# Performance work log

Measured on AMD Instinct MI355X. Metric: run time of the kernel, lower is better.

The kernel has to match this reference:

```python
import jax, jax.numpy as jnp
import numpy as np

H, TH, NH, NL, NB = 512, 768, 8, 12, 2
NE, NU, NI, NNZ, K, B = 16000, 2000, 4000, 40000, 10, 64
MD = H // 2
GAMA = 0.1


def _prelu(x, a):
    return jnp.where(x >= 0, x, a * x)


def _spmm(r, c, v, X, n):
    # sparse [n, m] @ X: gather X rows by col index, scale, segment-sum by row.
    return jax.ops.segment_sum(v[:, None] * X[c], r, num_segments=n)


def _forward(systemid, adj_row, adj_col, itemid_set,
             token_embeds, adj_val, node_embeds, user_embedding,
             token_proj_w, token_proj_b, trans_w, trans_b, trans_t_w, trans_t_b,
             meta_w1, meta_b1, meta_w2, meta_b2, sim_w1, sim_w2,
             p1_w1, p1_b1, p1_w2, p1_b2, p2_w, p2_b, prelu_a):
    tok = token_embeds @ token_proj_w + token_proj_b               # [B, H]
    # grouped mean over rows sharing the same system id (vectorized segment-mean)
    same = (systemid[:, None] == systemid[None, :]).astype(tok.dtype)
    group_mean = (same @ tok) / same.sum(1, keepdims=True)         # [B, H]
    filt = _prelu(group_mean @ trans_w + trans_b, prelu_a) * group_mean
    h = jax.nn.relu(filt @ meta_w1 + meta_b1)
    mapping = (h @ meta_w2 + meta_b2).reshape(B, H, H)             # per-sample hypernet weights
    enhanced = jnp.einsum('bh,bhk->bk', user_embedding[systemid], mapping)
    all_tok = user_embedding.at[systemid].set(enhanced)            # [NU, H]
    tok_edge = jnp.zeros_like(user_embedding).at[systemid].set(group_mean)
    # similarity between (enhanced) user/token reps and item reps
    u_rep = all_tok @ sim_w1
    i_rep = node_embeds[itemid_set] @ sim_w2
    u_n = u_rep / jnp.maximum(jnp.linalg.norm(u_rep, axis=1, keepdims=True), 1e-12)
    i_n = i_rep / jnp.maximum(jnp.linalg.norm(i_rep, axis=1, keepdims=True), 1e-12)
    sim = jax.nn.sigmoid(u_n @ i_n.T)                              # [NU, NI]
    tv, ti = jax.lax.top_k(sim, K)
    # combined sparse adjacency = original COO + per-user top-k added edges
    rows = jnp.concatenate([adj_row, jnp.repeat(jnp.arange(NU), K)])
    cols = jnp.concatenate([adj_col, itemid_set[ti].reshape(-1)])
    vals = jnp.concatenate([adj_val, tv.reshape(-1)])
    v_u = vals / jax.ops.segment_sum(vals, rows, num_segments=NU)[rows]   # row-normalized user->item
    v_i = vals / jax.ops.segment_sum(vals, cols, num_segments=NE)[cols]   # row-normalized item->user
    # LightGCN-style 2-layer propagation with multiplicative token gating
    user_tok = _prelu(tok_edge @ trans_t_w + trans_t_b, prelu_a) * tok_edge
    u0, i0 = all_tok, node_embeds
    Ai0 = _spmm(rows, cols, v_u, i0, NU)
    u1 = Ai0 + Ai0 * user_tok
    Att = _spmm(cols, rows, v_i, user_tok, NE)
    i1 = _spmm(cols, rows, v_i, u0, NE) + Att * i0
    Ai1 = _spmm(rows, cols, v_u, i1, NU)
    u2 = Ai1 + Ai1 * user_tok
    i2 = _spmm(cols, rows, v_i, u1, NE) + Att * i1
    user_final = (u0 + u1 + u2) / 3.0
    item_final = (i0 + i1 + i2) / 3.0
    # reconstruction loss vs dense adjacency restricted to item columns
    inv = jnp.full((NE,), -1, jnp.int32).at[itemid_set].set(jnp.arange(NI, dtype=jnp.int32))
    icol = inv[adj_col]
    valid = (icol >= 0).astype(sim.dtype)
    dense = jnp.zeros((NU, NI), sim.dtype).at[adj_row, jnp.maximum(icol, 0)].add(adj_val * valid)
    loss = GAMA * jnp.mean((sim - dense) ** 2)
    # prefix-prompt projection from per-batch system embeddings
    sys_final = user_final[systemid][:, None, :]                   # [B, 1, H]
    p1 = jax.nn.relu(sys_final @ p1_w1 + p1_b1) @ p1_w2 + p1_b2 + sys_final
    p2 = p1 @ p2_w + p2_b
    prompt = p2.reshape(B, 1, NL, NB, NH, H // NH).transpose(2, 3, 0, 4, 1, 5)
    return prompt, item_final, loss


def setup_inputs():
    ks = jax.random.split(jax.random.key(0), 20)
    rng = np.random.default_rng(0)
    s = 0.02
    itemid_set = jnp.asarray(np.sort(rng.choice(NE, NI, replace=False)).astype(np.int32))
    user_embedding = (s * jax.random.normal(ks[4], (NU, H), jnp.float32)).at[0].set(0.0)
    return {
        'systemid': jax.random.randint(ks[0], (B,), 0, NU),
        'adj_row': jax.random.randint(ks[1], (NNZ,), 0, NU),
        'adj_col': jax.random.randint(ks[2], (NNZ,), 0, NE),
        'itemid_set': itemid_set,
        'token_embeds': jax.random.normal(ks[3], (B, TH), jnp.float32),
        'adj_val': jnp.ones((NNZ,), jnp.float32),
        'node_embeds': s * jax.random.normal(ks[5], (NE, H), jnp.float32),
        'user_embedding': user_embedding,
        'token_proj_w': s * jax.random.normal(ks[6], (TH, H), jnp.float32),
        'token_proj_b': jnp.zeros((H,), jnp.float32),
        'trans_w': s * jax.random.normal(ks[7], (H, H), jnp.float32),
        'trans_b': jnp.zeros((H,), jnp.float32),
        'trans_t_w': s * jax.random.normal(ks[8], (H, H), jnp.float32),
        'trans_t_b': jnp.zeros((H,), jnp.float32),
        'meta_w1': s * jax.random.normal(ks[9], (H, MD), jnp.float32),
        'meta_b1': jnp.zeros((MD,), jnp.float32),
        'meta_w2': s * jax.random.normal(ks[10], (MD, H * H), jnp.float32),
        'meta_b2': jnp.zeros((H * H,), jnp.float32),
        'sim_w1': jax.random.normal(ks[11], (H, H), jnp.float32),
        'sim_w2': jax.random.normal(ks[12], (H, H), jnp.float32),
        'p1_w1': s * jax.random.normal(ks[13], (H, MD), jnp.float32),
        'p1_b1': jnp.zeros((MD,), jnp.float32),
        'p1_w2': s * jax.random.normal(ks[14], (MD, H), jnp.float32),
        'p1_b2': jnp.zeros((H,), jnp.float32),
        'p2_w': s * jax.random.normal(ks[15], (H, NL * NB * H), jnp.float32),
        'p2_b': jnp.zeros((NL * NB * H,), jnp.float32),
        'prelu_a': jnp.array(0.25, jnp.float32),
    }


def reference(systemid, adj_row, adj_col, itemid_set, token_embeds, adj_val,
              node_embeds, user_embedding, token_proj_w, token_proj_b,
              trans_w, trans_b, trans_t_w, trans_t_b,
              meta_w1, meta_b1, meta_w2, meta_b2, sim_w1, sim_w2,
              p1_w1, p1_b1, p1_w2, p1_b2, p2_w, p2_b, prelu_a):
    return _forward(systemid, adj_row, adj_col, itemid_set, token_embeds, adj_val,
                    node_embeds, user_embedding, token_proj_w, token_proj_b,
                    trans_w, trans_b, trans_t_w, trans_t_b,
                    meta_w1, meta_b1, meta_w2, meta_b2, sim_w1, sim_w2,
                    p1_w1, p1_b1, p1_w2, p1_b2, p2_w, p2_b, prelu_a)
```

## Files before the change

### kernel.cpp

```cpp
#include <hip/hip_runtime.h>

#define H     512
#define THD   768
#define MDIM  256
#define NE    16000
#define NU    2000
#define NI    4000
#define NNZ   40000
#define KTOP  10
#define NBATCH 64
#define NEDGE 60000
#define GAMA  0.1f
#define P2N   12288
#define PROMPT_N 786432
#define NLOSSB 2048

__device__ __forceinline__ float sigmoidf(float x){ return 1.0f/(1.0f+expf(-x)); }
__device__ __forceinline__ float4 f4z(){ return make_float4(0.f,0.f,0.f,0.f); }

__device__ __forceinline__ void gll16(const float* g, float* l){
  __builtin_amdgcn_global_load_lds(
      (const __attribute__((address_space(1))) void*)g,
      (__attribute__((address_space(3))) void*)l, 16, 0, 0);
}

__global__ void k_tok(const float* __restrict__ A, const float* __restrict__ W,
                      const float* __restrict__ bias, float* __restrict__ C){
  int b=blockIdx.x, c=blockIdx.y*256+threadIdx.x;
  const float* a=A+b*THD; float s=bias[c];
  for(int k=0;k<THD;k++) s+=a[k]*W[k*H+c];
  C[b*H+c]=s;
}

__global__ void k_gm(const int* __restrict__ sysid, const float* __restrict__ tok,
                     float* __restrict__ gm){
  int b=blockIdx.x, c=blockIdx.y*256+threadIdx.x;
  int sid=sysid[b]; float s=0.f, cnt=0.f;
  for(int j=0;j<NBATCH;j++){ if(sysid[j]==sid){ s+=tok[j*H+c]; cnt+=1.f; } }
  gm[b*H+c]=s/cnt;
}

__global__ __launch_bounds__(512) void k_front(const int* __restrict__ sysid,
        const float* __restrict__ gm,
        const float* __restrict__ trans_w, const float* __restrict__ trans_b,
        const float* __restrict__ mw1, const float* __restrict__ mb1,
        const float* __restrict__ ue, const float* __restrict__ mb2,
        const float* __restrict__ trt_w, const float* __restrict__ trt_b,
        const float* __restrict__ pa,
        float* __restrict__ hh, float* __restrict__ ueT, float* __restrict__ enh,
        float* __restrict__ usertok){
  __shared__ float fl[512];
  __shared__ float hp[512];
  int b=blockIdx.x, t=threadIdx.x, which=blockIdx.y;
  if(which==0){
    const float* g=gm+b*H;
    float s=trans_b[t];
    for(int k=0;k<H;k++) s+=g[k]*trans_w[k*H+t];
    float al=pa[0]; float pr=(s>=0.f)? s : al*s;
    fl[t]=pr*g[t];
    __syncthreads();
    int m=t&255, half=t>>8;
    float s2=0.f; int k0=half*256;
    for(int k=0;k<256;k++) s2+=fl[k0+k]*mw1[(k0+k)*MDIM+m];
    hp[t]=s2;
    __syncthreads();
    if(t<256) hh[b*MDIM+t]=fmaxf(hp[t]+hp[t+256]+mb1[t],0.f);
  } else if(which==1){
    const float* u=ue+(size_t)sysid[b]*H;
    float v=u[t];
    ueT[t*64+b]=v;
    float s=0.f;
    for(int h=0;h<H;h++) s+=u[h]*mb2[(size_t)h*H+t];
    enh[b*H+t]=s;
  } else {
    const float* a=gm+b*H; float s=trt_b[t];
    for(int k=0;k<H;k++) s+=a[k]*trt_w[k*H+t];
    float al=pa[0]; float pr=(s>=0.f)? s : al*s;
    usertok[(size_t)sysid[b]*H+t]=pr*gm[b*H+t];
  }
}

#define HCH 8
__global__ __launch_bounds__(128) void k_big(const float* __restrict__ hh,
        const float* __restrict__ ueT, const float* __restrict__ w2,
        float* __restrict__ partials){
  __shared__ float a_lds[2][HCH][64];
  __shared__ float w_lds[2][HCH][256];
  int m=blockIdx.x;
  int kt=blockIdx.y&1, hs=blockIdx.y>>1;
  int k0=kt*256;
  int hbase=hs*256;
  int t=threadIdx.x;
  int kg=t&15, bg=t>>4;
  const float* w2m = w2 + (size_t)m*(size_t)(H*H);

  float4 acc[8][4];
  #pragma unroll
  for(int r=0;r<8;r++){
    #pragma unroll
    for(int c=0;c<4;c++) acc[r][c]=f4z();
  }

  #define STAGE(buf,hc) do{                                             \
    int h0=hbase+(hc)*HCH;                                              \
    gll16(ueT + (size_t)(h0+(t>>4))*64 + (t&15)*4,                      \
          &a_lds[buf][t>>4][(t&15)*4]);                                 \
    _Pragma("unroll")                                                   \
    for(int j=0;j<4;j++){                                               \
      int i=t+j*128;                                                    \
      gll16(w2m + (size_t)(h0+(i>>6))*H + k0 + (i&63)*4,                \
            &w_lds[buf][i>>6][(i&63)*4]);                               \
    }                                                                   \
  }while(0)

  STAGE(0,0);
  int cur=0;
  for(int hc=0;hc<32;hc++){
    __syncthreads();
    if(hc<31) STAGE(cur^1,hc+1);
    #pragma unroll
    for(int hl=0;hl<HCH;hl++){
      float4 aL=*(const float4*)&a_lds[cur][hl][bg*4];
      float4 aH=*(const float4*)&a_lds[cur][hl][32+bg*4];
      float4 w0=*(const float4*)&w_lds[cur][hl][kg*4];
      float4 w1=*(const float4*)&w_lds[cur][hl][64+kg*4];
      float4 w2v=*(const float4*)&w_lds[cur][hl][128+kg*4];
      float4 w3=*(const float4*)&w_lds[cur][hl][192+kg*4];
      #define FMA4(ac,av,wv) ac.x+=(av)*wv.x; ac.y+=(av)*wv.y; ac.z+=(av)*wv.z; ac.w+=(av)*wv.w;
      #define ROWC(r,av) FMA4(acc[r][0],av,w0) FMA4(acc[r][1],av,w1) FMA4(acc[r][2],av,w2v) FMA4(acc[r][3],av,w3)
      ROWC(0,aL.x) ROWC(1,aL.y) ROWC(2,aL.z) ROWC(3,aL.w)
      ROWC(4,aH.x) ROWC(5,aH.y) ROWC(6,aH.z) ROWC(7,aH.w)
      #undef ROWC
      #undef FMA4
    }
    cur^=1;
  }
  int slice=hs*256+m;
  #pragma unroll
  for(int r=0;r<8;r++){
    int br=(r<4)? (bg*4+r) : (32+bg*4+(r-4));
    float hv=hh[br*MDIM+m];
    float* p=partials+((size_t)slice*NBATCH+br)*H+k0+kg*4;
    *(float4*)(p)    =make_float4(acc[r][0].x*hv,acc[r][0].y*hv,acc[r][0].z*hv,acc[r][0].w*hv);
    *(float4*)(p+64) =make_float4(acc[r][1].x*hv,acc[r][1].y*hv,acc[r][1].z*hv,acc[r][1].w*hv);
    *(float4*)(p+128)=make_float4(acc[r][2].x*hv,acc[r][2].y*hv,acc[r][2].z*hv,acc[r][2].w*hv);
    *(float4*)(p+192)=make_float4(acc[r][3].x*hv,acc[r][3].y*hv,acc[r][3].z*hv,acc[r][3].w*hv);
  }
  #undef STAGE
}

__global__ void k_red1(const float* __restrict__ partials, float* __restrict__ partial2){
  int idx=blockIdx.x*256+threadIdx.x;
  int g=idx>>15, col=idx&32767;
  const float* p=partials+(size_t)g*16*32768+col;
  float s=0.f;
  #pragma unroll
  for(int m=0;m<16;m++) s+=p[(size_t)m*32768];
  partial2[idx]=s;
}
__global__ void k_red2s(const int* __restrict__ sysid, const float* __restrict__ partial2,
                        const float* __restrict__ enh, float* __restrict__ alltok){
  int idx=blockIdx.x*256+threadIdx.x;
  int b=idx>>9, k=idx&511;
  float s=enh[idx];
  #pragma unroll
  for(int g=0;g<32;g++) s+=partial2[(size_t)g*32768+idx];
  alltok[(size_t)sysid[b]*H+k]=s;
}

template<int EPI, bool NT, bool AIDX>
__device__ __forceinline__ void gemm_body(float (*As)[68], float (*Bs)[68],
        const float* __restrict__ A, const float* __restrict__ Bm,
        const float* __restrict__ bias, const int* __restrict__ aidx,
        float* __restrict__ C, int M, int N, int K, int bx, int by){
  int n0=bx*64, m0=by*64;
  int t=threadIdx.x;
  int tn=t&15, tm=t>>4;
  float4 pa[2], pb[2];
  #pragma unroll
  for(int i=0;i<2;i++){
    int idx=t+i*256; int r=idx>>3, q=idx&7;
    int grow=m0+r;
    pa[i]=f4z();
    if(grow<M){
      const float* arow=A+(size_t)(AIDX? aidx[grow]:grow)*K;
      pa[i]=*(const float4*)(arow+q*4);
    }
  }
  #pragma unroll
  for(int i=0;i<2;i++){
    if(!NT){
      int idx=t+i*256; int r=idx>>4, q=idx&15;
      pb[i]=*(const float4*)(Bm+(size_t)r*N+n0+q*4);
    } else {
      int idx=t+i*256; int r=idx>>3, q=idx&7;
      int gn=n0+r;
      pb[i]=f4z();
      if(gn<N) pb[i]=*(const float4*)(Bm+(size_t)gn*K+q*4);
    }
  }
  float acc[4][4]={};
  for(int kt=0;kt<K;kt+=32){
    __syncthreads();
    #pragma unroll
    for(int i=0;i<2;i++){
      int idx=t+i*256; int r=idx>>3, q=idx&7;
      As[q*4+0][r]=pa[i].x; As[q*4+1][r]=pa[i].y; As[q*4+2][r]=pa[i].z; As[q*4+3][r]=pa[i].w;
    }
    #pragma unroll
    for(int i=0;i<2;i++){
      if(!NT){
        int idx=t+i*256; int r=idx>>4, q=idx&15;
        *(float4*)&Bs[r][q*4]=pb[i];
      } else {
        int idx=t+i*256; int r=idx>>3, q=idx&7;
        Bs[q*4+0][r]=pb[i].x; Bs[q*4+1][r]=pb[i].y; Bs[q*4+2][r]=pb[i].z; Bs[q*4+3][r]=pb[i].w;
      }
    }
    __syncthreads();
    if(kt+32<K){
      #pragma unroll
      for(int i=0;i<2;i++){
        int idx=t+i*256; int r=idx>>3, q=idx&7;
        int grow=m0+r;
        pa[i]=f4z();
        if(grow<M){
          const float* arow=A+(size_t)(AIDX? aidx[grow]:grow)*K;
          pa[i]=*(const float4*)(arow+kt+32+q*4);
        }
      }
      #pragma unroll
      for(int i=0;i<2;i++){
        if(!NT){
          int idx=t+i*256; int r=idx>>4, q=idx&15;
          pb[i]=*(const float4*)(Bm+(size_t)(kt+32+r)*N+n0+q*4);
        } else {
          int idx=t+i*256; int r=idx>>3, q=idx&7;
          int gn=n0+r;
          pb[i]=f4z();
          if(gn<N) pb[i]=*(const float4*)(Bm+(size_t)gn*K+kt+32+q*4);
        }
      }
    }
    #pragma unroll 8
    for(int k=0;k<32;k++){
      float4 a4=*(const float4*)&As[k][tm*4];
      float4 b4=*(const float4*)&Bs[k][tn*4];
      acc[0][0]+=a4.x*b4.x; acc[0][1]+=a4.x*b4.y; acc[0][2]+=a4.x*b4.z; acc[0][3]+=a4.x*b4.w;
      acc[1][0]+=a4.y*b4.x; acc[1][1]+=a4.y*b4.y; acc[1][2]+=a4.y*b4.z; acc[1][3]+=a4.y*b4.w;
      acc[2][0]+=a4.z*b4.x; acc[2][1]+=a4.z*b4.y; acc[2][2]+=a4.z*b4.z; acc[2][3]+=a4.z*b4.w;
      acc[3][0]+=a4.w*b4.x; acc[3][1]+=a4.w*b4.y; acc[3][2]+=a4.w*b4.z; acc[3][3]+=a4.w*b4.w;
    }
  }
  #pragma unroll
  for(int bi=0;bi<4;bi++){
    int row=m0+tm*4+bi; if(row>=M) continue;
    #pragma unroll
    for(int ki=0;ki<4;ki++){
      int col=n0+tn*4+ki; if(col>=N) continue;
      float v=acc[bi][ki];
      if(EPI==0){ if(bias) v+=bias[col]; }
      else { v=sigmoidf(v); }
      C[(size_t)row*N+col]=v;
    }
  }
}

template<int EPI, bool NT, bool AIDX>
__global__ __launch_bounds__(256) void k_gemm(const float* __restrict__ A,
        const float* __restrict__ Bm, const float* __restrict__ bias,
        const int* __restrict__ aidx, float* __restrict__ C, int M, int N, int K){
  __shared__ float As[32][68];
  __shared__ float Bs[32][68];
  gemm_body<EPI,NT,AIDX>(As,Bs,A,Bm,bias,aidx,C,M,N,K,blockIdx.x,blockIdx.y);
}

__global__ __launch_bounds__(256) void k_gemm_ui(const float* __restrict__ alltok,
        const float* __restrict__ node_emb, const float* __restrict__ sw1,
        const float* __restrict__ sw2, const int* __restrict__ itemid,
        float* __restrict__ urep, float* __restrict__ irep){
  __shared__ float As[32][68];
  __shared__ float Bs[32][68];
  if(blockIdx.y<32)
    gemm_body<0,false,false>(As,Bs,alltok,sw1,nullptr,nullptr,urep,NU,H,H,blockIdx.x,blockIdx.y);
  else
    gemm_body<0,false,true >(As,Bs,node_emb,sw2,nullptr,itemid,irep,NI,H,H,blockIdx.x,blockIdx.y-32);
}

__global__ __launch_bounds__(512) void k_gemm_sim(const float* __restrict__ A,
        const float* __restrict__ Bm, float* __restrict__ C, int M, int N){
  __shared__ float As[32][132];
  __shared__ float Bs[32][260];
  int n0=blockIdx.x*256, m0=blockIdx.y*128;
  int t=threadIdx.x;
  int tn=t&31, tm=t>>5;
  float4 pa[2], pb[4];
  #pragma unroll
  for(int i=0;i<2;i++){
    int idx=t+i*512; int r=idx>>3, q=idx&7;
    pa[i]=f4z();
    if(m0+r<M) pa[i]=*(const float4*)(A+(size_t)(m0+r)*H+q*4);
  }
  #pragma unroll
  for(int i=0;i<4;i++){
    int idx=t+i*512; int r=idx>>3, q=idx&7;
    pb[i]=f4z();
    if(n0+r<N) pb[i]=*(const float4*)(Bm+(size_t)(n0+r)*H+q*4);
  }
  float4 acc[8][2];
  #pragma unroll
  for(int r=0;r<8;r++){ acc[r][0]=f4z(); acc[r][1]=f4z(); }
  for(int kt=0;kt<H;kt+=32){
    __syncthreads();
    #pragma unroll
    for(int i=0;i<2;i++){
      int idx=t+i*512; int r=idx>>3, q=idx&7;
      As[q*4+0][r]=pa[i].x; As[q*4+1][r]=pa[i].y; As[q*4+2][r]=pa[i].z; As[q*4+3][r]=pa[i].w;
    }
    #pragma unroll
    for(int i=0;i<4;i++){
      int idx=t+i*512; int r=idx>>3, q=idx&7;
      Bs[q*4+0][r]=pb[i].x; Bs[q*4+1][r]=pb[i].y; Bs[q*4+2][r]=pb[i].z; Bs[q*4+3][r]=pb[i].w;
    }
    __syncthreads();
    if(kt+32<H){
      #pragma unroll
      for(int i=0;i<2;i++){
        int idx=t+i*512; int r=idx>>3, q=idx&7;
        pa[i]=f4z();
        if(m0+r<M) pa[i]=*(const float4*)(A+(size_t)(m0+r)*H+kt+32+q*4);
      }
      #pragma unroll
      for(int i=0;i<4;i++){
        int idx=t+i*512; int r=idx>>3, q=idx&7;
        pb[i]=f4z();
        if(n0+r<N) pb[i]=*(const float4*)(Bm+(size_t)(n0+r)*H+kt+32+q*4);
      }
    }
    #pragma unroll 8
    for(int k=0;k<32;k++){
      float4 a0=*(const float4*)&As[k][tm*4];
      float4 a1=*(const float4*)&As[k][64+tm*4];
      float4 b0=*(const float4*)&Bs[k][tn*4];
      float4 b1=*(const float4*)&Bs[k][128+tn*4];
      #define FMA4(ac,av,bv) ac.x+=(av)*bv.x; ac.y+=(av)*bv.y; ac.z+=(av)*bv.z; ac.w+=(av)*bv.w;
      #define ROW(r,av) FMA4(acc[r][0],av,b0) FMA4(acc[r][1],av,b1)
      ROW(0,a0.x) ROW(1,a0.y) ROW(2,a0.z) ROW(3,a0.w)
      ROW(4,a1.x) ROW(5,a1.y) ROW(6,a1.z) ROW(7,a1.w)
      #undef ROW
      #undef FMA4
    }
  }
  #pragma unroll
  for(int r=0;r<8;r++){
    int row=m0+((r<4)? (tm*4+r) : (64+tm*4+(r-4)));
    if(row>=M) continue;
    #pragma unroll
    for(int c=0;c<2;c++){
      int col0=n0+c*128+tn*4;
      float vv[4]={acc[r][c].x,acc[r][c].y,acc[r][c].z,acc[r][c].w};
      #pragma unroll
      for(int j=0;j<4;j++){
        int col=col0+j;
        if(col<N) C[(size_t)row*N+col]=sigmoidf(vv[j]);
      }
    }
  }
}

__global__ __launch_bounds__(256) void k_rownorm2(float* __restrict__ U, float* __restrict__ I){
  int r=blockIdx.x, t=threadIdx.x;
  float* X=(r<NU)? U+(size_t)r*H : I+(size_t)(r-NU)*H;
  float v1=X[t], v2=X[t+256];
  float ss=v1*v1+v2*v2;
  for(int o=32;o;o>>=1) ss+=__shfl_xor(ss,o);
  __shared__ float red[4];
  if((t&63)==0) red[t>>6]=ss;
  __syncthreads();
  float tot=red[0]+red[1]+red[2]+red[3];
  float nrm=fmaxf(sqrtf(tot),1e-12f);
  X[t]=v1/nrm; X[t+256]=v2/nrm;
}

__global__ __launch_bounds__(256) void k_topk(const float* __restrict__ sim,
        float* __restrict__ tv, int* __restrict__ ti){
  __shared__ float rv[4];
  __shared__ int   ri[4];
  int u=blockIdx.x, t=threadIdx.x;
  float v[16];
  #pragma unroll
  for(int j=0;j<16;j++){
    int gi=t+j*256;
    v[j]=(gi<NI)? sim[(size_t)u*NI+gi] : -1e30f;
  }
  for(int k=0;k<KTOP;k++){
    float bv=-1e30f; int bi=1<<30;
    #pragma unroll
    for(int j=0;j<16;j++){
      int gi=t+j*256;
      if(v[j]>bv){ bv=v[j]; bi=gi; }
    }
    #pragma unroll
    for(int o=32;o;o>>=1){
      float ov=__shfl_xor(bv,o); int oi=__shfl_xor(bi,o);
      if(ov>bv || (ov==bv && oi<bi)){ bv=ov; bi=oi; }
    }
    if((t&63)==0){ rv[t>>6]=bv; ri[t>>6]=bi; }
    __syncthreads();
    float fv=rv[0]; int fi=ri[0];
    #pragma unroll
    for(int w=1;w<4;w++){
      float ov=rv[w]; int oi=ri[w];
      if(ov>fv || (ov==fv && oi<fi)){ fv=ov; fi=oi; }
    }
    if(t==0){ tv[u*KTOP+k]=fv; ti[u*KTOP+k]=fi; }
    int jj=fi>>8, tt=fi&255;
    #pragma unroll
    for(int j=0;j<16;j++) if(tt==t && j==jj) v[j]=-1e30f;
    __syncthreads();
  }
}

__global__ void k_edges(const int* __restrict__ adj_row, const int* __restrict__ adj_col,
        const float* __restrict__ adj_val, const int* __restrict__ itemid,
        const float* __restrict__ tv, const int* __restrict__ ti,
        int* __restrict__ rows, int* __restrict__ cols, float* __restrict__ vals,
        float* __restrict__ seg_r, float* __restrict__ seg_c,
        int* __restrict__ row_cnt, int* __restrict__ col_cnt, int* __restrict__ inv){
  int e=blockIdx.x*256+threadIdx.x; if(e>=NEDGE) return;
  if(e<NI) inv[itemid[e]]=e;
  int r,c; float v;
  if(e<NNZ){ r=adj_row[e]; c=adj_col[e]; v=adj_val[e]; }
  else { int x=e-NNZ; int u=x/KTOP; r=u; c=itemid[ti[x]]; v=tv[x]; }
  rows[e]=r; cols[e]=c; vals[e]=v;
  atomicAdd(&seg_r[r],v); atomicAdd(&seg_c[c],v);
  atomicAdd(&row_cnt[r],1); atomicAdd(&col_cnt[c],1);
}

__global__ __launch_bounds__(1024) void k_scan(const int* __restrict__ rc, int* __restrict__ rp,
        const int* __restrict__ cc, int* __restrict__ cp){
  const int* cnt; int* ptr; int n;
  if(blockIdx.x==0){ cnt=rc; ptr=rp; n=NU; } else { cnt=cc; ptr=cp; n=NE; }
  int t=threadIdx.x;
  int chunk=(n+1023)>>10;
  int base=t*chunk;
  int s=0;
  for(int i=0;i<chunk;i++){ int j=base+i; if(j<n) s+=cnt[j]; }
  __shared__ int buf[1024];
  buf[t]=s; __syncthreads();
  for(int off=1;off<1024;off<<=1){
    int y=(t>=off)? buf[t-off]:0;
    __syncthreads();
    buf[t]+=y;
    __syncthreads();
  }
  int run=buf[t]-s;
  for(int i=0;i<chunk;i++){ int j=base+i; if(j<n){ ptr[j]=run; run+=cnt[j]; } }
  if(t==1023) ptr[n]=buf[1023];
}

__global__ void k_fill(const int* __restrict__ rows, const int* __restrict__ cols,
        const float* __restrict__ vals,
        const int* __restrict__ row_ptr, const int* __restrict__ col_ptr,
        const float* __restrict__ seg_r, const float* __restrict__ seg_c,
        int* __restrict__ fr, int* __restrict__ fc,
        int* __restrict__ ebr, int* __restrict__ ebc,
        float* __restrict__ v_u, float* __restrict__ v_i,
        const int* __restrict__ inv, float* __restrict__ dense){
  int e=blockIdx.x*256+threadIdx.x; if(e>=NEDGE) return;
  int r=rows[e], c=cols[e];
  ebr[row_ptr[r]+atomicAdd(&fr[r],1)]=e;
  ebc[col_ptr[c]+atomicAdd(&fc[c],1)]=e;
  v_u[e]=vals[e]/seg_r[r];
  v_i[e]=vals[e]/seg_c[c];
  if(e<NNZ){
    int ic=inv[c];
    if(ic>=0) atomicAdd(&dense[(size_t)r*NI+ic],vals[e]);
  }
}

__device__ __forceinline__ void spmm_u_body(int u, const int* __restrict__ row_ptr,
        const int* __restrict__ ebr, const int* __restrict__ cols,
        const float* __restrict__ v_u, const float* __restrict__ X,
        const float* __restrict__ usertok, float* __restrict__ out,
        int* sc, float* sv, float (*red)[512]){
  int t=threadIdx.x, w=t>>6, l=t&63;
  int s=row_ptr[u], n=row_ptr[u+1]-s;
  float4 a0=f4z(), a1=f4z();
  for(int base=0;base<n;base+=128){
    int cnt=min(n-base,128);
    if(t<cnt){ int e=ebr[s+base+t]; sc[t]=cols[e]; sv[t]=v_u[e]; }
    __syncthreads();
    for(int j=w;j<cnt;j+=4){
      float v=sv[j];
      const float4* xr=(const float4*)(X+(size_t)sc[j]*H);
      float4 x0=xr[l], x1=xr[l+64];
      a0.x+=v*x0.x; a0.y+=v*x0.y; a0.z+=v*x0.z; a0.w+=v*x0.w;
      a1.x+=v*x1.x; a1.y+=v*x1.y; a1.z+=v*x1.z; a1.w+=v*x1.w;
    }
    __syncthreads();
  }
  if(w>0){ *(float4*)&red[w-1][l*4]=a0; *(float4*)&red[w-1][l*4+256]=a1; }
  __syncthreads();
  if(w==0){
    #pragma unroll
    for(int ww=0;ww<3;ww++){
      float4 r0=*(const float4*)&red[ww][l*4], r1=*(const float4*)&red[ww][l*4+256];
      a0.x+=r0.x; a0.y+=r0.y; a0.z+=r0.z; a0.w+=r0.w;
      a1.x+=r1.x; a1.y+=r1.y; a1.z+=r1.z; a1.w+=r1.w;
    }
    const float4* ut=(const float4*)(usertok+(size_t)u*H);
    float4 u0=ut[l], u1=ut[l+64];
    float4* o=(float4*)(out+(size_t)u*H);
    o[l]   =make_float4(a0.x+a0.x*u0.x, a0.y+a0.y*u0.y, a0.z+a0.z*u0.z, a0.w+a0.w*u0.w);
    o[l+64]=make_float4(a1.x+a1.x*u1.x, a1.y+a1.y*u1.y, a1.z+a1.z*u1.z, a1.w+a1.w*u1.w);
  }
}

__device__ __forceinline__ void spmm_i1_body(int ib, const int* __restrict__ col_ptr,
        const int* __restrict__ ebc, const int* __restrict__ rows,
        const float* __restrict__ v_i, const float* __restrict__ alltok,
        const float* __restrict__ usertok, const float* __restrict__ i0,
        float* __restrict__ Att, float* __restrict__ i1){
  int i=ib*4+(threadIdx.x>>6);
  int l=threadIdx.x&63;
  int s=col_ptr[i], e1=col_ptr[i+1];
  float4 aA0=f4z(),aA1=f4z(),aU0=f4z(),aU1=f4z();
  for(int j=s;j<e1;j++){
    int e=ebc[j]; float v=v_i[e]; int r=rows[e];
    const float4* ur=(const float4*)(usertok+(size_t)r*H);
    const float4* ar=(const float4*)(alltok+(size_t)r*H);
    float4 u0=ur[l],u1v=ur[l+64],A0=ar[l],A1=ar[l+64];
    aA0.x+=v*u0.x; aA0.y+=v*u0.y; aA0.z+=v*u0.z; aA0.w+=v*u0.w;
    aA1.x+=v*u1v.x; aA1.y+=v*u1v.y; aA1.z+=v*u1v.z; aA1.w+=v*u1v.w;
    aU0.x+=v*A0.x; aU0.y+=v*A0.y; aU0.z+=v*A0.z; aU0.w+=v*A0.w;
    aU1.x+=v*A1.x; aU1.y+=v*A1.y; aU1.z+=v*A1.z; aU1.w+=v*A1.w;
  }
  size_t o=(size_t)i*128;
  const float4* z=(const float4*)i0;
  float4 z0=z[o+l], z1=z[o+l+64];
  ((float4*)Att)[o+l]   =aA0;
  ((float4*)Att)[o+l+64]=aA1;
  ((float4*)i1)[o+l]   =make_float4(aU0.x+aA0.x*z0.x, aU0.y+aA0.y*z0.y, aU0.z+aA0.z*z0.z, aU0.w+aA0.w*z0.w);
  ((float4*)i1)[o+l+64]=make_float4(aU1.x+aA1.x*z1.x, aU1.y+aA1.y*z1.y, aU1.z+aA1.z*z1.z, aU1.w+aA1.w*z1.w);
}

__device__ __forceinline__ void spmm_i2_body(int ib, const int* __restrict__ col_ptr,
        const int* __restrict__ ebc, const int* __restrict__ rows,
        const float* __restrict__ v_i, const float* __restrict__ u1,
        const float* __restrict__ Att, const float* __restrict__ i1,
        const float* __restrict__ i0, float* __restrict__ item_out){
  int i=ib*4+(threadIdx.x>>6);
  int l=threadIdx.x&63;
  int s=col_ptr[i], e1=col_ptr[i+1];
  float4 a0=f4z(), a1=f4z();
  for(int j=s;j<e1;j++){
    int e=ebc[j]; float v=v_i[e];
    const float4* ur=(const float4*)(u1+(size_t)rows[e]*H);
    float4 x0=ur[l], x1=ur[l+64];
    a0.x+=v*x0.x; a0.y+=v*x0.y; a0.z+=v*x0.z; a0.w+=v*x0.w;
    a1.x+=v*x1.x; a1.y+=v*x1.y; a1.z+=v*x1.z; a1.w+=v*x1.w;
  }
  size_t o=(size_t)i*128;
  float4 A0=((const float4*)Att)[o+l], A1=((const float4*)Att)[o+l+64];
  float4 I0=((const float4*)i1)[o+l],  I1=((const float4*)i1)[o+l+64];
  float4 Z0=((const float4*)i0)[o+l],  Z1=((const float4*)i0)[o+l+64];
  float4 r0=make_float4((Z0.x+I0.x+a0.x+A0.x*I0.x)/3.f,(Z0.y+I0.y+a0.y+A0.y*I0.y)/3.f,
                        (Z0.z+I0.z+a0.z+A0.z*I0.z)/3.f,(Z0.w+I0.w+a0.w+A0.w*I0.w)/3.f);
  float4 r1=make_float4((Z1.x+I1.x+a1.x+A1.x*I1.x)/3.f,(Z1.y+I1.y+a1.y+A1.y*I1.y)/3.f,
                        (Z1.z+I1.z+a1.z+A1.z*I1.z)/3.f,(Z1.w+I1.w+a1.w+A1.w*I1.w)/3.f);
  ((float4*)item_out)[o+l]=r0;
  ((float4*)item_out)[o+l+64]=r1;
}

__device__ __forceinline__ void loss_body(int lb, const float* __restrict__ sim,
        const float* __restrict__ dense, float* __restrict__ acc, float* red){
  int t=threadIdx.x;
  size_t n4=(size_t)NU*NI/4;
  float s=0.f;
  for(size_t i=(size_t)lb*256+t; i<n4; i+=(size_t)NLOSSB*256){
    float4 a=((const float4*)sim)[i], d=((const float4*)dense)[i];
    float dx=a.x-d.x, dy=a.y-d.y, dz=a.z-d.z, dw=a.w-d.w;
    s+=dx*dx+dy*dy+dz*dz+dw*dw;
  }
  red[t]=s; __syncthreads();
  for(int o=128;o;o>>=1){ if(t<o) red[t]+=red[t+o]; __syncthreads(); }
  if(t==0) atomicAdd(acc,red[0]);
}

__global__ __launch_bounds__(256) void k_stage1(const int* __restrict__ row_ptr,
        const int* __restrict__ ebr, const int* __restrict__ colsA,
        const float* __restrict__ v_u, const float* __restrict__ node_emb,
        const float* __restrict__ usertok, float* __restrict__ u1,
        const int* __restrict__ col_ptr, const int* __restrict__ ebc,
        const int* __restrict__ rowsA, const float* __restrict__ v_i,
        const float* __restrict__ alltok, float* __restrict__ Att, float* __restrict__ i1,
        const float* __restrict__ sim, const float* __restrict__ dense,
        float* __restrict__ loss_acc){
  __shared__ int   sc[128];
  __shared__ float sv[128];
  __shared__ float red[3][512];
  int bid=blockIdx.x;
  if(bid<NU)              spmm_u_body(bid,row_ptr,ebr,colsA,v_u,node_emb,usertok,u1,sc,sv,red);
  else if(bid<NU+NE/4)    spmm_i1_body(bid-NU,col_ptr,ebc,rowsA,v_i,alltok,usertok,node_emb,Att,i1);
  else                    loss_body(bid-(NU+NE/4),sim,dense,loss_acc,(float*)red);
}

__global__ __launch_bounds__(256) void k_stage2(const int* __restrict__ row_ptr,
        const int* __restrict__ ebr, const int* __restrict__ colsA,
        const float* __restrict__ v_u, const float* __restrict__ i1,
        const float* __restrict__ usertok, float* __restrict__ u2,
        const int* __restrict__ col_ptr, const int* __restrict__ ebc,
        const int* __restrict__ rowsA, const float* __restrict__ v_i,
        const float* __restrict__ u1, const float* __restrict__ Att,
        const float* __restrict__ node_emb, float* __restrict__ item_out,
        const float* __restrict__ loss_acc, float* __restrict__ out_loss){
  __shared__ int   sc[128];
  __shared__ float sv[128];
  __shared__ float red[3][512];
  int bid=blockIdx.x;
  if(bid<NU) spmm_u_body(bid,row_ptr,ebr,colsA,v_u,i1,usertok,u2,sc,sv,red);
  else if(bid<NU+NE/4) spmm_i2_body(bid-NU,col_ptr,ebc,rowsA,v_i,u1,Att,i1,node_emb,item_out);
  else if(threadIdx.x==0) out_loss[0]=GAMA*(loss_acc[0]/(float)((size_t)NU*NI));
}

__global__ __launch_bounds__(512) void k_sysq_p1(const int* __restrict__ sysid,
        const float* __restrict__ u0, const float* __restrict__ u1, const float* __restrict__ u2,
        const float* __restrict__ p1w1, const float* __restrict__ p1b1,
        const float* __restrict__ p1w2, const float* __restrict__ p1b2,
        float* __restrict__ p1buf){
  __shared__ float sf[512];
  __shared__ float hp[512];
  __shared__ float qv[256];
  int b=blockIdx.x, t=threadIdx.x;
  size_t o=(size_t)sysid[b]*H+t;
  float sfv=(u0[o]+u1[o]+u2[o])/3.0f;
  sf[t]=sfv;
  __syncthreads();
  int m=t&255, half=t>>8;
  float s=0.f; int k0=half*256;
  for(int k=0;k<256;k++) s+=sf[k0+k]*p1w1[(k0+k)*MDIM+m];
  hp[t]=s;
  __syncthreads();
  if(t<256) qv[t]=fmaxf(hp[t]+hp[t+256]+p1b1[t],0.f);
  __syncthreads();
  float s2=p1b2[t];
  for(int k=0;k<256;k++) s2+=qv[k]*p1w2[k*H+t];
  p1buf[b*H+t]=s2+sf[t];
}

__global__ void k_perm(const float* __restrict__ p2, float* __restrict__ out){
  int idx=blockIdx.x*256+threadIdx.x;
  int x=idx&511;
  int b=(idx>>9)&63;
  int c=idx>>15;
  out[idx]=p2[(size_t)b*P2N+c*512+x];
}

extern "C" void kernel_launch(void* const* d_in, const int* in_sizes, int n_in,
                              void* d_out, int out_size, void* d_ws, size_t ws_size,
                              hipStream_t stream){
  const int*   sysid   =(const int*)  d_in[0];
  const int*   adj_row =(const int*)  d_in[1];
  const int*   adj_col =(const int*)  d_in[2];
  const int*   itemid  =(const int*)  d_in[3];
  const float* tok_emb =(const float*)d_in[4];
  const float* adj_val =(const float*)d_in[5];
  const float* node_emb=(const float*)d_in[6];
  const float* user_emb=(const float*)d_in[7];
  const float* tp_w    =(const float*)d_in[8];
  const float* tp_b    =(const float*)d_in[9];
  const float* trans_w =(const float*)d_in[10];
  const float* trans_b =(const float*)d_in[11];
  const float* trt_w   =(const float*)d_in[12];
  const float* trt_b   =(const float*)d_in[13];
  const float* mw1     =(const float*)d_in[14];
  const float* mb1     =(const float*)d_in[15];
  const float* mw2     =(const float*)d_in[16];
  const float* mb2     =(const float*)d_in[17];
  const float* sw1     =(const float*)d_in[18];
  const float* sw2     =(const float*)d_in[19];
  const float* p1w1    =(const float*)d_in[20];
  const float* p1b1    =(const float*)d_in[21];
  const float* p1w2    =(const float*)d_in[22];
  const float* p1b2    =(const float*)d_in[23];
  const float* p2w     =(const float*)d_in[24];
  const float* p2b     =(const float*)d_in[25];
  const float* pa      =(const float*)d_in[26];

  float* out_prompt=(float*)d_out;
  float* out_item  =out_prompt+PROMPT_N;
  float* out_loss  =out_item+(size_t)NE*H;

  char* ws=(char*)d_ws; size_t off=0;
  auto A=[&](size_t bytes)->char*{ char* p=ws+off; off+=(bytes+255)&~(size_t)255; return p; };
  float* tok     =(float*)A((size_t)NBATCH*H*4);
  float* gm      =(float*)A((size_t)NBATCH*H*4);
  float* hh      =(float*)A((size_t)NBATCH*MDIM*4);
  float* ueT     =(float*)A((size_t)H*NBATCH*4);
  float* enh     =(float*)A((size_t)NBATCH*H*4);
  float* irep    =(float*)A((size_t)NI*H*4);
  float* alltok  =(float*)A((size_t)NU*H*4);
  float* urep    =(float*)A((size_t)NU*H*4);
  float* u1      =(float*)A((size_t)NU*H*4);
  float* u2      =(float*)A((size_t)NU*H*4);
  float* partials=(float*)A((size_t)512*NBATCH*H*4);
  float* partial2=(float*)A((size_t)32*32768*4);
  float* sim     =(float*)A((size_t)NU*NI*4);
  float* dense   =(float*)A((size_t)NU*NI*4);
  float* Att     =(float*)A((size_t)NE*H*4);
  float* i1      =(float*)A((size_t)NE*H*4);
  float* tv      =(float*)A((size_t)NU*KTOP*4);
  int*   ti      =(int*)  A((size_t)NU*KTOP*4);
  int*   rowsA   =(int*)  A((size_t)NEDGE*4);
  int*   colsA   =(int*)  A((size_t)NEDGE*4);
  float* valsA   =(float*)A((size_t)NEDGE*4);
  float* v_u     =(float*)A((size_t)NEDGE*4);
  float* v_i     =(float*)A((size_t)NEDGE*4);
  int*   ebr     =(int*)  A((size_t)NEDGE*4);
  int*   ebc     =(int*)  A((size_t)NEDGE*4);
  int*   row_ptr =(int*)  A((size_t)(NU+1)*4);
  int*   col_ptr =(int*)  A((size_t)(NE+1)*4);
  size_t zb_bytes=(size_t)NU*H*4 + (size_t)(NU+NE)*4*3 + 256;
  char*  zb      =A(zb_bytes);
  float* usertok =(float*)zb;
  float* seg_r   =usertok+(size_t)NU*H;
  float* seg_c   =seg_r+NU;
  int*   row_cnt =(int*)(seg_c+NE);
  int*   col_cnt =row_cnt+NU;
  int*   fr      =col_cnt+NE;
  int*   fc      =fr+NU;
  float* loss_acc=(float*)(fc+NE);
  int*   inv     =(int*)  A((size_t)NE*4);
  float* p1buf   =(float*)A((size_t)NBATCH*H*4);
  float* p2buf   =(float*)A((size_t)NBATCH*P2N*4);
  (void)ws_size; (void)n_in; (void)in_sizes; (void)out_size;

  hipMemcpyAsync(alltok,user_emb,(size_t)NU*H*4,hipMemcpyDeviceToDevice,stream);
  hipMemsetAsync(zb,0,zb_bytes,stream);
  hipMemsetAsync(inv,0xFF,(size_t)NE*4,stream);
  hipMemsetAsync(dense,0,(size_t)NU*NI*4,stream);

  k_tok  <<<dim3(NBATCH,2),256,0,stream>>>(tok_emb,tp_w,tp_b,tok);
  k_gm   <<<dim3(NBATCH,2),256,0,stream>>>(sysid,tok,gm);
  k_front<<<dim3(NBATCH,3),512,0,stream>>>(sysid,gm,trans_w,trans_b,mw1,mb1,
                                           user_emb,mb2,trt_w,trt_b,pa,
                                           hh,ueT,enh,usertok);
  k_big  <<<dim3(256,4),128,0,stream>>>(hh,ueT,mw2,partials);
  k_red1 <<<4096,256,0,stream>>>(partials,partial2);
  k_red2s<<<128,256,0,stream>>>(sysid,partial2,enh,alltok);

  k_gemm_ui<<<dim3(8,95),256,0,stream>>>(alltok,node_emb,sw1,sw2,itemid,urep,irep);
  k_rownorm2<<<NU+NI,256,0,stream>>>(urep,irep);
  k_gemm_sim<<<dim3(16,16),512,0,stream>>>(urep,irep,sim,NU,NI);
  k_topk<<<NU,256,0,stream>>>(sim,tv,ti);

  k_edges<<<(NEDGE+255)/256,256,0,stream>>>(adj_row,adj_col,adj_val,itemid,tv,ti,
                                            rowsA,colsA,valsA,seg_r,seg_c,row_cnt,col_cnt,inv);
  k_scan<<<2,1024,0,stream>>>(row_cnt,row_ptr,col_cnt,col_ptr);
  k_fill<<<(NEDGE+255)/256,256,0,stream>>>(rowsA,colsA,valsA,row_ptr,col_ptr,seg_r,seg_c,
                                           fr,fc,ebr,ebc,v_u,v_i,inv,dense);

  k_stage1<<<NU+NE/4+NLOSSB,256,0,stream>>>(row_ptr,ebr,colsA,v_u,node_emb,usertok,u1,
                                            col_ptr,ebc,rowsA,v_i,alltok,Att,i1,
                                            sim,dense,loss_acc);

  k_stage2<<<NU+NE/4+1,256,0,stream>>>(row_ptr,ebr,colsA,v_u,i1,usertok,u2,
                                       col_ptr,ebc,rowsA,v_i,u1,Att,node_emb,out_item,
                                       loss_acc,out_loss);

  k_sysq_p1<<<NBATCH,512,0,stream>>>(sysid,alltok,u1,u2,p1w1,p1b1,p1w2,p1b2,p1buf);
  k_gemm<0,false,false><<<dim3(192,1),256,0,stream>>>(p1buf,p2w,p2b,nullptr,p2buf,NBATCH,P2N,H);
  k_perm<<<PROMPT_N/256,256,0,stream>>>(p2buf,out_prompt);
}
```

Before: 698.5 us.

## Fold group mean into token projection and overlap user/item GEMM with front stage

The token projection and grouped mean are merged into one kernel that averages the raw token embeddings before projecting them, using the linearity of the projection. The user and item representation GEMM now runs on the original user embeddings in the same launch as the hypernetwork front stage. Only the batch rows that receive enhanced embeddings are then recomputed and normalized in a small fix-up kernel, and row normalization is folded into the first reduction kernel. This removes several launches and takes the big GEMM off the serial chain, at the cost of some recomputation and a tie between correctness and the order in which kernels overwrite rows.

```diff
diff --git a/kernel.cpp b/kernel.cpp
--- a/kernel.cpp
+++ b/kernel.cpp
@@ -24,157 +24,32 @@
       (__attribute__((address_space(3))) void*)l, 16, 0, 0);
 }
 
-__global__ void k_tok(const float* __restrict__ A, const float* __restrict__ W,
-                      const float* __restrict__ bias, float* __restrict__ C){
-  int b=blockIdx.x, c=blockIdx.y*256+threadIdx.x;
-  const float* a=A+b*THD; float s=bias[c];
-  for(int k=0;k<THD;k++) s+=a[k]*W[k*H+c];
-  C[b*H+c]=s;
-}
-
-__global__ void k_gm(const int* __restrict__ sysid, const float* __restrict__ tok,
-                     float* __restrict__ gm){
-  int b=blockIdx.x, c=blockIdx.y*256+threadIdx.x;
-  int sid=sysid[b]; float s=0.f, cnt=0.f;
-  for(int j=0;j<NBATCH;j++){ if(sysid[j]==sid){ s+=tok[j*H+c]; cnt+=1.f; } }
-  gm[b*H+c]=s/cnt;
-}
-
-__global__ __launch_bounds__(512) void k_front(const int* __restrict__ sysid,
-        const float* __restrict__ gm,
-        const float* __restrict__ trans_w, const float* __restrict__ trans_b,
-        const float* __restrict__ mw1, const float* __restrict__ mb1,
-        const float* __restrict__ ue, const float* __restrict__ mb2,
-        const float* __restrict__ trt_w, const float* __restrict__ trt_b,
-        const float* __restrict__ pa,
-        float* __restrict__ hh, float* __restrict__ ueT, float* __restrict__ enh,
-        float* __restrict__ usertok){
-  __shared__ float fl[512];
-  __shared__ float hp[512];
-  int b=blockIdx.x, t=threadIdx.x, which=blockIdx.y;
-  if(which==0){
-    const float* g=gm+b*H;
-    float s=trans_b[t];
-    for(int k=0;k<H;k++) s+=g[k]*trans_w[k*H+t];
-    float al=pa[0]; float pr=(s>=0.f)? s : al*s;
-    fl[t]=pr*g[t];
-    __syncthreads();
-    int m=t&255, half=t>>8;
-    float s2=0.f; int k0=half*256;
-    for(int k=0;k<256;k++) s2+=fl[k0+k]*mw1[(k0+k)*MDIM+m];
-    hp[t]=s2;
-    __syncthreads();
-    if(t<256) hh[b*MDIM+t]=fmaxf(hp[t]+hp[t+256]+mb1[t],0.f);
-  } else if(which==1){
-    const float* u=ue+(size_t)sysid[b]*H;
-    float v=u[t];
-    ueT[t*64+b]=v;
-    float s=0.f;
-    for(int h=0;h<H;h++) s+=u[h]*mb2[(size_t)h*H+t];
-    enh[b*H+t]=s;
-  } else {
-    const float* a=gm+b*H; float s=trt_b[t];
-    for(int k=0;k<H;k++) s+=a[k]*trt_w[k*H+t];
-    float al=pa[0]; float pr=(s>=0.f)? s : al*s;
-    usertok[(size_t)sysid[b]*H+t]=pr*gm[b*H+t];
-  }
-}
-
-#define HCH 8
-__global__ __launch_bounds__(128) void k_big(const float* __restrict__ hh,
-        const float* __restrict__ ueT, const float* __restrict__ w2,
-        float* __restrict__ partials){
-  __shared__ float a_lds[2][HCH][64];
-  __shared__ float w_lds[2][HCH][256];
-  int m=blockIdx.x;
-  int kt=blockIdx.y&1, hs=blockIdx.y>>1;
-  int k0=kt*256;
-  int hbase=hs*256;
-  int t=threadIdx.x;
-  int kg=t&15, bg=t>>4;
-  const float* w2m = w2 + (size_t)m*(size_t)(H*H);
-
-  float4 acc[8][4];
-  #pragma unroll
-  for(int r=0;r<8;r++){
-    #pragma unroll
-    for(int c=0;c<4;c++) acc[r][c]=f4z();
-  }
-
-  #define STAGE(buf,hc) do{                                             \
-    int h0=hbase+(hc)*HCH;                                              \
-    gll16(ueT + (size_t)(h0+(t>>4))*64 + (t&15)*4,                      \
-          &a_lds[buf][t>>4][(t&15)*4]);                                 \
-    _Pragma("unroll")                                                   \
-    for(int j=0;j<4;j++){                                               \
-      int i=t+j*128;                                                    \
-      gll16(w2m + (size_t)(h0+(i>>6))*H + k0 + (i&63)*4,                \
-            &w_lds[buf][i>>6][(i&63)*4]);                               \
-    }                                                                   \
-  }while(0)
-
-  STAGE(0,0);
-  int cur=0;
-  for(int hc=0;hc<32;hc++){
-    __syncthreads();
-    if(hc<31) STAGE(cur^1,hc+1);
-    #pragma unroll
-    for(int hl=0;hl<HCH;hl++){
-      float4 aL=*(const float4*)&a_lds[cur][hl][bg*4];
-      float4 aH=*(const float4*)&a_lds[cur][hl][32+bg*4];
-      float4 w0=*(const float4*)&w_lds[cur][hl][kg*4];
-      float4 w1=*(const float4*)&w_lds[cur][hl][64+kg*4];
-      float4 w2v=*(const float4*)&w_lds[cur][hl][128+kg*4];
-      float4 w3=*(const float4*)&w_lds[cur][hl][192+kg*4];
-      #define FMA4(ac,av,wv) ac.x+=(av)*wv.x; ac.y+=(av)*wv.y; ac.z+=(av)*wv.z; ac.w+=(av)*wv.w;
-      #define ROWC(r,av) FMA4(acc[r][0],av,w0) FMA4(acc[r][1],av,w1) FMA4(acc[r][2],av,w2v) FMA4(acc[r][3],av,w3)
-      ROWC(0,aL.x) ROWC(1,aL.y) ROWC(2,aL.z) ROWC(3,aL.w)
-      ROWC(4,aH.x) ROWC(5,aH.y) ROWC(6,aH.z) ROWC(7,aH.w)
-      #undef ROWC
-      #undef FMA4
-    }
-    cur^=1;
-  }
-  int slice=hs*256+m;
-  #pragma unroll
-  for(int r=0;r<8;r++){
-    int br=(r<4)? (bg*4+r) : (32+bg*4+(r-4));
-    float hv=hh[br*MDIM+m];
-    float* p=partials+((size_t)slice*NBATCH+br)*H+k0+kg*4;
-    *(float4*)(p)    =make_float4(acc[r][0].x*hv,acc[r][0].y*hv,acc[r][0].z*hv,acc[r][0].w*hv);
-    *(float4*)(p+64) =make_float4(acc[r][1].x*hv,acc[r][1].y*hv,acc[r][1].z*hv,acc[r][1].w*hv);
-    *(float4*)(p+128)=make_float4(acc[r][2].x*hv,acc[r][2].y*hv,acc[r][2].z*hv,acc[r][2].w*hv);
-    *(float4*)(p+192)=make_float4(acc[r][3].x*hv,acc[r][3].y*hv,acc[r][3].z*hv,acc[r][3].w*hv);
-  }
-  #undef STAGE
-}
-
-__global__ void k_red1(const float* __restrict__ partials, float* __restrict__ partial2){
-  int idx=blockIdx.x*256+threadIdx.x;
-  int g=idx>>15, col=idx&32767;
-  const float* p=partials+(size_t)g*16*32768+col;
-  float s=0.f;
-  #pragma unroll
-  for(int m=0;m<16;m++) s+=p[(size_t)m*32768];
-  partial2[idx]=s;
-}
-__global__ void k_red2s(const int* __restrict__ sysid, const float* __restrict__ partial2,
-                        const float* __restrict__ enh, float* __restrict__ alltok){
-  int idx=blockIdx.x*256+threadIdx.x;
-  int b=idx>>9, k=idx&511;
-  float s=enh[idx];
-  #pragma unroll
-  for(int g=0;g<32;g++) s+=partial2[(size_t)g*32768+idx];
-  alltok[(size_t)sysid[b]*H+k]=s;
+__global__ __launch_bounds__(256) void k_gmd(const int* __restrict__ sysid,
+        const float* __restrict__ A, const float* __restrict__ W,
+        const float* __restrict__ bias, float* __restrict__ gm){
+  __shared__ float ma[THD];
+  int b=blockIdx.x, half=blockIdx.y, t=threadIdx.x;
+  int sid=sysid[b];
+  #pragma unroll
+  for(int j3=0;j3<3;j3++){
+    int k=t+j3*256;
+    float s=0.f, cnt=0.f;
+    for(int j=0;j<NBATCH;j++){ if(sysid[j]==sid){ s+=A[j*THD+k]; cnt+=1.f; } }
+    ma[k]=s/cnt;
+  }
+  __syncthreads();
+  int c=half*256+t;
+  float s=bias[c];
+  for(int k=0;k<THD;k++) s+=ma[k]*W[k*H+c];
+  gm[b*H+c]=s;
 }
 
 template<int EPI, bool NT, bool AIDX>
 __device__ __forceinline__ void gemm_body(float (*As)[68], float (*Bs)[68],
         const float* __restrict__ A, const float* __restrict__ Bm,
         const float* __restrict__ bias, const int* __restrict__ aidx,
-        float* __restrict__ C, int M, int N, int K, int bx, int by){
+        float* __restrict__ C, int M, int N, int K, int bx, int by, int t){
   int n0=bx*64, m0=by*64;
-  int t=threadIdx.x;
   int tn=t&15, tm=t>>4;
   float4 pa[2], pb[2];
   #pragma unroll
@@ -272,19 +147,184 @@
         const int* __restrict__ aidx, float* __restrict__ C, int M, int N, int K){
   __shared__ float As[32][68];
   __shared__ float Bs[32][68];
-  gemm_body<EPI,NT,AIDX>(As,Bs,A,Bm,bias,aidx,C,M,N,K,blockIdx.x,blockIdx.y);
-}
-
-__global__ __launch_bounds__(256) void k_gemm_ui(const float* __restrict__ alltok,
+  gemm_body<EPI,NT,AIDX>(As,Bs,A,Bm,bias,aidx,C,M,N,K,blockIdx.x,blockIdx.y,threadIdx.x);
+}
+
+__global__ __launch_bounds__(512) void k_launchA(const int* __restrict__ sysid,
+        const float* __restrict__ gm,
+        const float* __restrict__ trans_w, const float* __restrict__ trans_b,
+        const float* __restrict__ mw1, const float* __restrict__ mb1,
+        const float* __restrict__ ue, const float* __restrict__ mb2,
+        const float* __restrict__ trt_w, const float* __restrict__ trt_b,
+        const float* __restrict__ pa,
         const float* __restrict__ node_emb, const float* __restrict__ sw1,
         const float* __restrict__ sw2, const int* __restrict__ itemid,
-        float* __restrict__ urep, float* __restrict__ irep){
-  __shared__ float As[32][68];
-  __shared__ float Bs[32][68];
-  if(blockIdx.y<32)
-    gemm_body<0,false,false>(As,Bs,alltok,sw1,nullptr,nullptr,urep,NU,H,H,blockIdx.x,blockIdx.y);
-  else
-    gemm_body<0,false,true >(As,Bs,node_emb,sw2,nullptr,itemid,irep,NI,H,H,blockIdx.x,blockIdx.y-32);
+        float* __restrict__ hh, float* __restrict__ ueT, float* __restrict__ enh,
+        float* __restrict__ usertok, float* __restrict__ urep, float* __restrict__ irep){
+  __shared__ float As[2][32][68];
+  __shared__ float Bs[2][32][68];
+  int bid=blockIdx.x, t=threadIdx.x;
+  if(bid<192){
+    float* fl=(float*)As;
+    float* hp=((float*)As)+512;
+    int which=bid>>6, b=bid&63;
+    if(which==0){
+      const float* g=gm+b*H;
+      float s=trans_b[t];
+      for(int k=0;k<H;k++) s+=g[k]*trans_w[k*H+t];
+      float al=pa[0]; float pr=(s>=0.f)? s : al*s;
+      fl[t]=pr*g[t];
+      __syncthreads();
+      int m=t&255, half=t>>8;
+      float s2=0.f; int k0=half*256;
+      for(int k=0;k<256;k++) s2+=fl[k0+k]*mw1[(k0+k)*MDIM+m];
+      hp[t]=s2;
+      __syncthreads();
+      if(t<256) hh[b*MDIM+t]=fmaxf(hp[t]+hp[t+256]+mb1[t],0.f);
+    } else if(which==1){
+      const float* u=ue+(size_t)sysid[b]*H;
+      float v=u[t];
+      ueT[t*64+b]=v;
+      float s=0.f;
+      for(int h=0;h<H;h++) s+=u[h]*mb2[(size_t)h*H+t];
+      enh[b*H+t]=s;
+    } else {
+      const float* a=gm+b*H; float s=trt_b[t];
+      for(int k=0;k<H;k++) s+=a[k]*trt_w[k*H+t];
+      float al=pa[0]; float pr=(s>=0.f)? s : al*s;
+      usertok[(size_t)sysid[b]*H+t]=pr*gm[b*H+t];
+    }
+  } else {
+    int p=bid-192;
+    int h=t>>8, tid=t&255;
+    int tile=p*2+h;
+    int by=tile>>3, bx=tile&7;
+    if(by<32)
+      gemm_body<0,false,false>(As[h],Bs[h],ue,sw1,nullptr,nullptr,urep,NU,H,H,bx,by,tid);
+    else
+      gemm_body<0,false,true >(As[h],Bs[h],node_emb,sw2,nullptr,itemid,irep,NI,H,H,bx,by-32,tid);
+  }
+}
+
+#define HCH 8
+__global__ __launch_bounds__(128) void k_big(const float* __restrict__ hh,
+        const float* __restrict__ ueT, const float* __restrict__ w2,
+        float* __restrict__ partials){
+  __shared__ float a_lds[2][HCH][64];
+  __shared__ float w_lds[2][HCH][256];
+  int m=blockIdx.x;
+  int kt=blockIdx.y&1, hs=blockIdx.y>>1;
+  int k0=kt*256;
+  int hbase=hs*256;
+  int t=threadIdx.x;
+  int kg=t&15, bg=t>>4;
+  const float* w2m = w2 + (size_t)m*(size_t)(H*H);
+
+  float4 acc[8][4];
+  #pragma unroll
+  for(int r=0;r<8;r++){
+    #pragma unroll
+    for(int c=0;c<4;c++) acc[r][c]=f4z();
+  }
+
+  #define STAGE(buf,hc) do{                                             \
+    int h0=hbase+(hc)*HCH;                                              \
+    gll16(ueT + (size_t)(h0+(t>>4))*64 + (t&15)*4,                      \
+          &a_lds[buf][t>>4][(t&15)*4]);                                 \
+    _Pragma("unroll")                                                   \
+    for(int j=0;j<4;j++){                                               \
+      int i=t+j*128;                                                    \
+      gll16(w2m + (size_t)(h0+(i>>6))*H + k0 + (i&63)*4,                \
+            &w_lds[buf][i>>6][(i&63)*4]);                               \
+    }                                                                   \
+  }while(0)
+
+  STAGE(0,0);
+  int cur=0;
+  for(int hc=0;hc<32;hc++){
+    __syncthreads();
+    if(hc<31) STAGE(cur^1,hc+1);
+    #pragma unroll
+    for(int hl=0;hl<HCH;hl++){
+      float4 aL=*(const float4*)&a_lds[cur][hl][bg*4];
+      float4 aH=*(const float4*)&a_lds[cur][hl][32+bg*4];
+      float4 w0=*(const float4*)&w_lds[cur][hl][kg*4];
+      float4 w1=*(const float4*)&w_lds[cur][hl][64+kg*4];
+      float4 w2v=*(const float4*)&w_lds[cur][hl][128+kg*4];
+      float4 w3=*(const float4*)&w_lds[cur][hl][192+kg*4];
+      #define FMA4(ac,av,wv) ac.x+=(av)*wv.x; ac.y+=(av)*wv.y; ac.z+=(av)*wv.z; ac.w+=(av)*wv.w;
+      #define ROWC(r,av) FMA4(acc[r][0],av,w0) FMA4(acc[r][1],av,w1) FMA4(acc[r][2],av,w2v) FMA4(acc[r][3],av,w3)
+      ROWC(0,aL.x) ROWC(1,aL.y) ROWC(2,aL.z) ROWC(3,aL.w)
+      ROWC(4,aH.x) ROWC(5,aH.y) ROWC(6,aH.z) ROWC(7,aH.w)
+      #undef ROWC
+      #undef FMA4
+    }
+    cur^=1;
+  }
+  int slice=hs*256+m;
+  #pragma unroll
+  for(int r=0;r<8;r++){
+    int br=(r<4)? (bg*4+r) : (32+bg*4+(r-4));
+    float hv=hh[br*MDIM+m];
+    float* p=partials+((size_t)slice*NBATCH+br)*H+k0+kg*4;
+    *(float4*)(p)    =make_float4(acc[r][0].x*hv,acc[r][0].y*hv,acc[r][0].z*hv,acc[r][0].w*hv);
+    *(float4*)(p+64) =make_float4(acc[r][1].x*hv,acc[r][1].y*hv,acc[r][1].z*hv,acc[r][1].w*hv);
+    *(float4*)(p+128)=make_float4(acc[r][2].x*hv,acc[r][2].y*hv,acc[r][2].z*hv,acc[r][2].w*hv);
+    *(float4*)(p+192)=make_float4(acc[r][3].x*hv,acc[r][3].y*hv,acc[r][3].z*hv,acc[r][3].w*hv);
+  }
+  #undef STAGE
+}
+
+__global__ __launch_bounds__(256) void k_red1n(const float* __restrict__ partials,
+        float* __restrict__ partial2, float* __restrict__ urep, float* __restrict__ irep){
+  __shared__ float red4[4];
+  int bid=blockIdx.x, t=threadIdx.x;
+  if(bid<4096){
+    int idx=bid*256+t;
+    int g=idx>>15, col=idx&32767;
+    const float* p=partials+(size_t)g*16*32768+col;
+    float s=0.f;
+    #pragma unroll
+    for(int m=0;m<16;m++) s+=p[(size_t)m*32768];
+    partial2[idx]=s;
+  } else {
+    int r=bid-4096;
+    float* X=(r<NU)? urep+(size_t)r*H : irep+(size_t)(r-NU)*H;
+    float v1=X[t], v2=X[t+256];
+    float ss=v1*v1+v2*v2;
+    for(int o=32;o;o>>=1) ss+=__shfl_xor(ss,o);
+    if((t&63)==0) red4[t>>6]=ss;
+    __syncthreads();
+    float tot=red4[0]+red4[1]+red4[2]+red4[3];
+    float nrm=fmaxf(sqrtf(tot),1e-12f);
+    X[t]=v1/nrm; X[t+256]=v2/nrm;
+  }
+}
+
+__global__ __launch_bounds__(512) void k_red2p(const int* __restrict__ sysid,
+        const float* __restrict__ partial2, const float* __restrict__ enh,
+        const float* __restrict__ sw1, float* __restrict__ alltok,
+        float* __restrict__ urep){
+  __shared__ float ef[512];
+  __shared__ float rn[8];
+  int b=blockIdx.x, t=threadIdx.x;
+  int idx=b*512+t;
+  float s=enh[idx];
+  #pragma unroll
+  for(int g=0;g<32;g++) s+=partial2[(size_t)g*32768+idx];
+  ef[t]=s;
+  int uid=sysid[b];
+  alltok[(size_t)uid*H+t]=s;
+  __syncthreads();
+  float uv=0.f;
+  for(int k=0;k<H;k++) uv+=ef[k]*sw1[k*H+t];
+  float ss=uv*uv;
+  for(int o=32;o;o>>=1) ss+=__shfl_xor(ss,o);
+  if((t&63)==0) rn[t>>6]=ss;
+  __syncthreads();
+  float tot=rn[0]+rn[1]+rn[2]+rn[3]+rn[4]+rn[5]+rn[6]+rn[7];
+  float nrm=fmaxf(sqrtf(tot),1e-12f);
+  urep[(size_t)uid*H+t]=uv/nrm;
 }
 
 __global__ __launch_bounds__(512) void k_gemm_sim(const float* __restrict__ A,
@@ -366,20 +406,6 @@
       }
     }
   }
-}
-
-__global__ __launch_bounds__(256) void k_rownorm2(float* __restrict__ U, float* __restrict__ I){
-  int r=blockIdx.x, t=threadIdx.x;
-  float* X=(r<NU)? U+(size_t)r*H : I+(size_t)(r-NU)*H;
-  float v1=X[t], v2=X[t+256];
-  float ss=v1*v1+v2*v2;
-  for(int o=32;o;o>>=1) ss+=__shfl_xor(ss,o);
-  __shared__ float red[4];
-  if((t&63)==0) red[t>>6]=ss;
-  __syncthreads();
-  float tot=red[0]+red[1]+red[2]+red[3];
-  float nrm=fmaxf(sqrtf(tot),1e-12f);
-  X[t]=v1/nrm; X[t+256]=v2/nrm;
 }
 
 __global__ __launch_bounds__(256) void k_topk(const float* __restrict__ sim,
@@ -694,7 +720,6 @@
 
   char* ws=(char*)d_ws; size_t off=0;
   auto A=[&](size_t bytes)->char*{ char* p=ws+off; off+=(bytes+255)&~(size_t)255; return p; };
-  float* tok     =(float*)A((size_t)NBATCH*H*4);
   float* gm      =(float*)A((size_t)NBATCH*H*4);
   float* hh      =(float*)A((size_t)NBATCH*MDIM*4);
   float* ueT     =(float*)A((size_t)H*NBATCH*4);
@@ -741,17 +766,15 @@
   hipMemsetAsync(inv,0xFF,(size_t)NE*4,stream);
   hipMemsetAsync(dense,0,(size_t)NU*NI*4,stream);
 
-  k_tok  <<<dim3(NBATCH,2),256,0,stream>>>(tok_emb,tp_w,tp_b,tok);
-  k_gm   <<<dim3(NBATCH,2),256,0,stream>>>(sysid,tok,gm);
-  k_front<<<dim3(NBATCH,3),512,0,stream>>>(sysid,gm,trans_w,trans_b,mw1,mb1,
-                                           user_emb,mb2,trt_w,trt_b,pa,
-                                           hh,ueT,enh,usertok);
+  k_gmd<<<dim3(NBATCH,2),256,0,stream>>>(sysid,tok_emb,tp_w,tp_b,gm);
+  k_launchA<<<192+380,512,0,stream>>>(sysid,gm,trans_w,trans_b,mw1,mb1,
+                                      user_emb,mb2,trt_w,trt_b,pa,
+                                      node_emb,sw1,sw2,itemid,
+                                      hh,ueT,enh,usertok,urep,irep);
   k_big  <<<dim3(256,4),128,0,stream>>>(hh,ueT,mw2,partials);
-  k_red1 <<<4096,256,0,stream>>>(partials,partial2);
-  k_red2s<<<128,256,0,stream>>>(sysid,partial2,enh,alltok);
-
-  k_gemm_ui<<<dim3(8,95),256,0,stream>>>(alltok,node_emb,sw1,sw2,itemid,urep,irep);
-  k_rownorm2<<<NU+NI,256,0,stream>>>(urep,irep);
+  k_red1n<<<4096+NU+NI,256,0,stream>>>(partials,partial2,urep,irep);
+  k_red2p<<<NBATCH,512,0,stream>>>(sysid,partial2,enh,sw1,alltok,urep);
+
   k_gemm_sim<<<dim3(16,16),512,0,stream>>>(urep,irep,sim,NU,NI);
   k_topk<<<NU,256,0,stream>>>(sim,tv,ti);
 
```

Measured after the change: 709.9 us. About the same (+1.6%).
